# Performance work log

Hardware: AMD Instinct MI355X
Metric: run time of the kernel (lower is better)

Reference implementation:

```python
import jax, jax.numpy as jnp
import numpy as np

L, E, S, V, B, T = 6, 768, 1024, 32000, 2, 1024
FF = 4 * E
EPS = 1e-5

def _layernorm(v, w, b):
    m = jnp.mean(v, axis=-1, keepdims=True)
    var = jnp.mean((v - m) ** 2, axis=-1, keepdims=True)
    return (v - m) * jax.lax.rsqrt(var + EPS) * w + b

def setup_inputs() -> dict:
    key = jax.random.key(0)
    ks = jax.random.split(key, 12)
    s = 0.02
    n = lambda k, shp: (jax.random.normal(k, shp, jnp.float32) * s)
    return {
        "x": jax.random.randint(ks[0], (B, T), 0, V),
        "tok_emb": n(ks[1], (V, E)),
        "pos_emb": jax.random.normal(ks[2], (S, E), jnp.float32),  # nn.Parameter(randn)
        "Wq": n(ks[3], (L, E, E)), "bq": jnp.zeros((L, E), jnp.float32),
        "Wk": n(ks[4], (L, E, E)), "bk": jnp.zeros((L, E), jnp.float32),
        "Wv": n(ks[5], (L, E, E)), "bv": jnp.zeros((L, E), jnp.float32),
        "ln1w": jnp.ones((L, E), jnp.float32), "ln1b": jnp.zeros((L, E), jnp.float32),
        "W1": n(ks[6], (L, E, FF)), "b1": jnp.zeros((L, FF), jnp.float32),
        "W2": n(ks[7], (L, FF, E)), "b2": jnp.zeros((L, E), jnp.float32),
        "ln2w": jnp.ones((L, E), jnp.float32), "ln2b": jnp.zeros((L, E), jnp.float32),
        "Wo": n(ks[8], (E, V)), "bo": jnp.zeros((V,), jnp.float32),
    }

def reference(x, tok_emb, pos_emb, Wq, bq, Wk, bk, Wv, bv, ln1w, ln1b,
              W1, b1, W2, b2, ln2w, ln2b, Wo, bo):
    t = x.shape[1]
    h = tok_emb[x] + pos_emb[:t]  # [B,T,E]
    scale = jnp.sqrt(jnp.float32(E))
    tril = jnp.tril(jnp.ones((t, t), bool))

    def layer(h, p):
        wq, bq_, wk, bk_, wv, bv_, l1w, l1b, w1, b1_, w2, b2_, l2w, l2b = p
        Q = h @ wq + bq_
        K = h @ wk + bk_
        Vv = h @ wv + bv_
        scores = jnp.einsum('btd,bsd->bts', Q, K) / scale
        # original adds a mask of 1.0 on allowed positions, -inf elsewhere
        masked = jnp.where(tril, scores + 1.0, -jnp.inf)
        A = jax.nn.softmax(masked, axis=-1)
        att = jnp.einsum('bts,bsd->btd', A, Vv)
        h1 = _layernorm(h + att, l1w, l1b)
        ffn = jax.nn.relu(h1 @ w1 + b1_) @ w2 + b2_
        h2 = _layernorm(ffn + h1, l2w, l2b)
        return h2, None

    params = (Wq, bq, Wk, bk, Wv, bv, ln1w, ln1b, W1, b1, W2, b2, ln2w, ln2b)
    h, _ = jax.lax.scan(layer, h, params)
    return h @ Wo + bo  # [B,T,V]
```

## Files before the change

kernel.cpp:

```cpp
#include <hip/hip_runtime.h>
#include <stdint.h>

typedef __bf16 v8bf __attribute__((ext_vector_type(8)));
typedef float  v4f  __attribute__((ext_vector_type(4)));

__device__ __forceinline__ float bf2f(uint16_t h) {
    union { uint32_t u; float f; } x; x.u = ((uint32_t)h) << 16; return x.f;
}
__device__ __forceinline__ uint16_t f2bf(float f) {
    union { float f; uint32_t u; } x; x.f = f;
    uint32_t r = x.u + 0x7fffu + ((x.u >> 16) & 1u);
    return (uint16_t)(r >> 16);
}

__device__ __forceinline__ void gload16(const uint16_t* g, uint16_t* l) {
    __builtin_amdgcn_global_load_lds((const __attribute__((address_space(1))) void*)g,
                                     (__attribute__((address_space(3))) void*)l, 16, 0, 0);
}

__global__ void k_embed(const int* __restrict__ x, const float* __restrict__ tok,
                        const float* __restrict__ pos, float* __restrict__ hf,
                        uint16_t* __restrict__ hb)
{
    int i = blockIdx.x;
    int t = i & 1023;
    int tk = x[i];
    const float* te = tok + (long)tk * 768;
    const float* pe = pos + (long)t * 768;
    for (int j = threadIdx.x; j < 768; j += 256) {
        float v = te[j] + pe[j];
        hf[(long)i * 768 + j] = v;
        hb[(long)i * 768 + j] = f2bf(v);
    }
}

template<typename SrcT>
__global__ void k_transpose(const SrcT* __restrict__ src, uint16_t* __restrict__ dst,
                            int ldS, int ldD, long sBatch, long dBatch)
{
    __shared__ float tile[32][33];
    src += (long)blockIdx.z * sBatch;
    dst += (long)blockIdx.z * dBatch;
    int c0 = blockIdx.x * 32, r0 = blockIdx.y * 32;
    int tx = threadIdx.x, ty = threadIdx.y;
    #pragma unroll
    for (int i = 0; i < 4; ++i) {
        int r = r0 + ty + i * 8;
        SrcT s = src[(long)r * ldS + c0 + tx];
        float v;
        if constexpr (sizeof(SrcT) == 4) v = (float)s; else v = bf2f((uint16_t)s);
        tile[ty + i * 8][tx] = v;
    }
    __syncthreads();
    #pragma unroll
    for (int i = 0; i < 4; ++i) {
        int c = c0 + ty + i * 8;
        dst[(long)c * ldD + r0 + tx] = f2bf(tile[tx][ty + i * 8]);
    }
}

__global__ void k_concat3(const float* __restrict__ a, const float* __restrict__ b,
                          const float* __restrict__ c, float* __restrict__ out)
{
    int l = blockIdx.y;
    const float* s = (blockIdx.x == 0) ? a : ((blockIdx.x == 1) ? b : c);
    s += (long)l * 768;
    for (int j = threadIdx.x; j < 768; j += 256)
        out[(long)l * 2304 + blockIdx.x * 768 + j] = s[j];
}

template<typename OutT, int BN, bool BIAS, bool RELU, bool RES>
__global__ void k_gemm(const uint16_t* __restrict__ A, const uint16_t* __restrict__ BT,
                       OutT* __restrict__ C, const float* __restrict__ bias,
                       const float* __restrict__ res,
                       int K, int lda, int ldb, int ldc,
                       long bsA, long bsB, long bsC, float scale, int causal)
{
    constexpr int NT = BN / 32;
    const int nwg = gridDim.x * gridDim.y;
    int lin = blockIdx.y * gridDim.x + blockIdx.x;
    {
        int q = nwg >> 3, r = nwg & 7, x = lin & 7, i = lin >> 3;
        lin = (x < r ? x * (q + 1) : r * (q + 1) + (x - r) * q) + i;
    }
    const int mt = lin % gridDim.y;
    const int nt = lin / gridDim.y;

    if (causal == 1 && nt * BN >= (mt + 1) * 128) return;
    const int Keff = (causal == 2) ? ((mt + 1) * 128 < K ? (mt + 1) * 128 : K) : K;

    __shared__ uint16_t As[128 * 32];
    __shared__ uint16_t Bs[BN * 32];
    const int tid  = threadIdx.x;
    const int lane = tid & 63;
    const int bz   = blockIdx.z;
    const uint16_t* Ab = A + (long)bz * bsA + (long)mt * 128 * lda;
    const uint16_t* Bb = BT + (long)bz * bsB + (long)nt * BN * ldb;

    const int wm = (tid >> 6) >> 1, wn = (tid >> 6) & 1;
    const int fr = lane & 15, fq = lane >> 4;

    const int r0 = tid >> 2;
    const int s0 = (tid & 3) * 8;

    v4f acc[4][NT];
    #pragma unroll
    for (int m = 0; m < 4; ++m)
        #pragma unroll
        for (int n = 0; n < NT; ++n) acc[m][n] = (v4f){0.f, 0.f, 0.f, 0.f};

    for (int kt = 0; kt < Keff; kt += 32) {
        gload16(Ab + (long)r0 * lda + kt + s0,        &As[tid * 8]);
        gload16(Ab + (long)(r0 + 64) * lda + kt + s0, &As[2048 + tid * 8]);
        gload16(Bb + (long)r0 * ldb + kt + s0,        &Bs[tid * 8]);
        if constexpr (BN == 128)
            gload16(Bb + (long)(r0 + 64) * ldb + kt + s0, &Bs[2048 + tid * 8]);
        __syncthreads();
        v8bf ag[4], bg[NT];
        #pragma unroll
        for (int m = 0; m < 4; ++m)
            ag[m] = *(const v8bf*)&As[(wm * 64 + m * 16 + fr) * 32 + fq * 8];
        #pragma unroll
        for (int n = 0; n < NT; ++n)
            bg[n] = *(const v8bf*)&Bs[(wn * (BN / 2) + n * 16 + fr) * 32 + fq * 8];
        #pragma unroll
        for (int m = 0; m < 4; ++m)
            #pragma unroll
            for (int n = 0; n < NT; ++n)
                acc[m][n] = __builtin_amdgcn_mfma_f32_16x16x32_bf16(ag[m], bg[n], acc[m][n], 0, 0, 0);
        __syncthreads();
    }

    OutT* Cb = C + (long)bz * bsC + (long)mt * 128 * ldc + nt * BN;
    const float* Rb = RES ? (res + (long)bz * bsC + (long)mt * 128 * ldc + nt * BN) : nullptr;
    #pragma unroll
    for (int n = 0; n < NT; ++n) {
        int col = wn * (BN / 2) + n * 16 + fr;
        float bv = BIAS ? bias[nt * BN + col] : 0.f;
        #pragma unroll
        for (int m = 0; m < 4; ++m) {
            #pragma unroll
            for (int r = 0; r < 4; ++r) {
                int row = wm * 64 + m * 16 + fq * 4 + r;
                float v = acc[m][n][r] * scale + bv;
                if (RES) v += Rb[(long)row * ldc + col];
                if (RELU) v = fmaxf(v, 0.f);
                if constexpr (sizeof(OutT) == 4) Cb[(long)row * ldc + col] = v;
                else                             Cb[(long)row * ldc + col] = f2bf(v);
            }
        }
    }
}

__global__ __launch_bounds__(512, 2)
void k_gemm256(const uint16_t* __restrict__ A, const uint16_t* __restrict__ BT,
               float* __restrict__ C, const float* __restrict__ bias,
               int K, int lda, int ldb, int ldc, float scale)
{
    __shared__ uint16_t lds[4][2][8192];

    const int nwg = gridDim.x * gridDim.y;
    int lin = blockIdx.y * gridDim.x + blockIdx.x;
    {
        int q = nwg >> 3, r = nwg & 7, x = lin & 7, i = lin >> 3;
        lin = (x < r ? x * (q + 1) : r * (q + 1) + (x - r) * q) + i;
    }
    const int mt = lin % gridDim.y;
    const int nt = lin / gridDim.y;

    const int tid  = threadIdx.x;
    const int lane = tid & 63;
    const int wid  = tid >> 6;
    const int wm = wid >> 2, wn = wid & 3;
    const int fr = lane & 15, fq = lane >> 4;
    const int swz = (fq ^ (fr & 3)) * 8;

    const uint16_t* Ab = A  + (long)mt * 256 * lda;
    const uint16_t* Bb = BT + (long)nt * 256 * ldb;

    const int srow = tid >> 2;
    const int ssl  = ((tid & 3) ^ (srow & 3)) * 8;
    const int KT   = K >> 5;

    v4f acc[8][4];
    #pragma unroll
    for (int m = 0; m < 8; ++m)
        #pragma unroll
        for (int n = 0; n < 4; ++n) acc[m][n] = (v4f){0.f, 0.f, 0.f, 0.f};

    #pragma unroll
    for (int t = 0; t < 2; ++t) {
        gload16(Ab + (long)srow * lda + t * 32 + ssl,         &lds[t][0][tid * 8]);
        gload16(Ab + (long)(srow + 128) * lda + t * 32 + ssl, &lds[t][0][4096 + tid * 8]);
        gload16(Bb + (long)srow * ldb + t * 32 + ssl,         &lds[t][1][tid * 8]);
        gload16(Bb + (long)(srow + 128) * ldb + t * 32 + ssl, &lds[t][1][4096 + tid * 8]);
    }

    for (int kti = 0; kti < KT; ++kti) {
        const int ring = kti & 3;
        const uint16_t* lA = &lds[ring][0][0];
        const uint16_t* lB = &lds[ring][1][0];
        uint16_t* sA = &lds[(ring + 2) & 3][0][0];
        uint16_t* sB = &lds[(ring + 2) & 3][1][0];
        const int koff = (kti + 2) * 32;
        const bool more = (kti + 2) < KT;

        if (kti + 1 < KT) asm volatile("s_waitcnt vmcnt(4)" ::: "memory");
        else              asm volatile("s_waitcnt vmcnt(0)" ::: "memory");
        __builtin_amdgcn_s_barrier();

        v8bf bfr[4], a0[4];
        #pragma unroll
        for (int n = 0; n < 4; ++n)
            bfr[n] = *(const v8bf*)&lB[(wn * 64 + n * 16 + fr) * 32 + swz];
        #pragma unroll
        for (int m = 0; m < 4; ++m)
            a0[m] = *(const v8bf*)&lA[(wm * 128 + m * 16 + fr) * 32 + swz];
        if (more) {
            gload16(Ab + (long)srow * lda + koff + ssl,         &sA[tid * 8]);
            gload16(Ab + (long)(srow + 128) * lda + koff + ssl, &sA[4096 + tid * 8]);
        }
        __builtin_amdgcn_s_setprio(1);
        #pragma unroll
        for (int m = 0; m < 4; ++m)
            #pragma unroll
            for (int n = 0; n < 4; ++n)
                acc[m][n] = __builtin_amdgcn_mfma_f32_16x16x32_bf16(a0[m], bfr[n], acc[m][n], 0, 0, 0);
        __builtin_amdgcn_s_setprio(0);

        __builtin_amdgcn_s_barrier();
        v8bf a1[4];
        #pragma unroll
        for (int m = 0; m < 4; ++m)
            a1[m] = *(const v8bf*)&lA[(wm * 128 + (m + 4) * 16 + fr) * 32 + swz];
        if (more) {
            gload16(Bb + (long)srow * ldb + koff + ssl,         &sB[tid * 8]);
            gload16(Bb + (long)(srow + 128) * ldb + koff + ssl, &sB[4096 + tid * 8]);
        }
        __builtin_amdgcn_s_setprio(1);
        #pragma unroll
        for (int m = 0; m < 4; ++m)
            #pragma unroll
            for (int n = 0; n < 4; ++n)
                acc[m + 4][n] = __builtin_amdgcn_mfma_f32_16x16x32_bf16(a1[m], bfr[n], acc[m + 4][n], 0, 0, 0);
        __builtin_amdgcn_s_setprio(0);
    }

    float* Cb = C + (long)(mt * 256 + wm * 128) * ldc + nt * 256 + wn * 64;
    #pragma unroll
    for (int n = 0; n < 4; ++n) {
        int col = n * 16 + fr;
        float bv = bias[nt * 256 + wn * 64 + col];
        #pragma unroll
        for (int m = 0; m < 8; ++m) {
            #pragma unroll
            for (int r = 0; r < 4; ++r) {
                int row = m * 16 + fq * 4 + r;
                Cb[(long)row * ldc + col] = acc[m][n][r] * scale + bv;
            }
        }
    }
}

__global__ void k_softmax(const float* __restrict__ S, uint16_t* __restrict__ P)
{
    int t = blockIdx.x, b = blockIdx.y;
    const float* row = S + ((long)b * 1024 + t) * 1024;
    uint16_t* pr = P + ((long)b * 1024 + t) * 1024;
    int limit = (t & ~127) + 128;
    int s0 = threadIdx.x * 4;
    float vals[4] = {0.f, 0.f, 0.f, 0.f};
    if (s0 < limit) {
        float4 vv = *(const float4*)(row + s0);
        vals[0] = vv.x; vals[1] = vv.y; vals[2] = vv.z; vals[3] = vv.w;
    }
    float mx = -1e30f;
    #pragma unroll
    for (int j = 0; j < 4; ++j) if (s0 + j <= t) mx = fmaxf(mx, vals[j]);
    #pragma unroll
    for (int o = 32; o; o >>= 1) mx = fmaxf(mx, __shfl_xor(mx, o));
    __shared__ float red[8];
    int wave = threadIdx.x >> 6, lane = threadIdx.x & 63;
    if (lane == 0) red[wave] = mx;
    __syncthreads();
    mx = fmaxf(fmaxf(red[0], red[1]), fmaxf(red[2], red[3]));
    float e[4]; float sum = 0.f;
    #pragma unroll
    for (int j = 0; j < 4; ++j) { e[j] = (s0 + j <= t) ? __expf(vals[j] - mx) : 0.f; sum += e[j]; }
    #pragma unroll
    for (int o = 32; o; o >>= 1) sum += __shfl_xor(sum, o);
    if (lane == 0) red[4 + wave] = sum;
    __syncthreads();
    sum = red[4] + red[5] + red[6] + red[7];
    float inv = 1.f / sum;
    if (s0 < limit) {
        #pragma unroll
        for (int j = 0; j < 4; ++j) pr[s0 + j] = f2bf(e[j] * inv);
    }
}

__global__ void k_ln(const float* __restrict__ a,
                     const float* __restrict__ w, const float* __restrict__ bias,
                     float* __restrict__ outf, uint16_t* __restrict__ outb)
{
    int row = blockIdx.x;
    const float* ar = a + (long)row * 768;
    float v[3]; float s1 = 0.f, s2 = 0.f;
    #pragma unroll
    for (int i = 0; i < 3; ++i) {
        int e = threadIdx.x + i * 256;
        v[i] = ar[e];
        s1 += v[i]; s2 += v[i] * v[i];
    }
    #pragma unroll
    for (int o = 32; o; o >>= 1) { s1 += __shfl_xor(s1, o); s2 += __shfl_xor(s2, o); }
    __shared__ float red[8];
    int wave = threadIdx.x >> 6, lane = threadIdx.x & 63;
    if (lane == 0) { red[wave] = s1; red[4 + wave] = s2; }
    __syncthreads();
    s1 = red[0] + red[1] + red[2] + red[3];
    s2 = red[4] + red[5] + red[6] + red[7];
    float mean = s1 * (1.f / 768.f);
    float var  = s2 * (1.f / 768.f) - mean * mean;
    float rstd = rsqrtf(var + 1e-5f);
    #pragma unroll
    for (int i = 0; i < 3; ++i) {
        int e = threadIdx.x + i * 256;
        float o = (v[i] - mean) * rstd * w[e] + bias[e];
        outf[(long)row * 768 + e] = o;
        outb[(long)row * 768 + e] = f2bf(o);
    }
}

__global__ void k_ln_ffn2(const float* __restrict__ p, long pstride,
                          const float* __restrict__ b2, const float* __restrict__ h1,
                          const float* __restrict__ w, const float* __restrict__ bias,
                          float* __restrict__ outf, uint16_t* __restrict__ outb)
{
    int row = blockIdx.x;
    long base = (long)row * 768;
    float v[3]; float s1 = 0.f, s2 = 0.f;
    #pragma unroll
    for (int i = 0; i < 3; ++i) {
        int e = threadIdx.x + i * 256;
        float acc = b2[e] + h1[base + e];
        #pragma unroll
        for (int s = 0; s < 4; ++s) acc += p[base + e + s * pstride];
        v[i] = acc;
        s1 += acc; s2 += acc * acc;
    }
    #pragma unroll
    for (int o = 32; o; o >>= 1) { s1 += __shfl_xor(s1, o); s2 += __shfl_xor(s2, o); }
    __shared__ float red[8];
    int wave = threadIdx.x >> 6, lane = threadIdx.x & 63;
    if (lane == 0) { red[wave] = s1; red[4 + wave] = s2; }
    __syncthreads();
    s1 = red[0] + red[1] + red[2] + red[3];
    s2 = red[4] + red[5] + red[6] + red[7];
    float mean = s1 * (1.f / 768.f);
    float var  = s2 * (1.f / 768.f) - mean * mean;
    float rstd = rsqrtf(var + 1e-5f);
    #pragma unroll
    for (int i = 0; i < 3; ++i) {
        int e = threadIdx.x + i * 256;
        float o = (v[i] - mean) * rstd * w[e] + bias[e];
        outf[base + e] = o;
        outb[base + e] = f2bf(o);
    }
}

extern "C" void kernel_launch(void* const* d_in, const int* in_sizes, int n_in,
                              void* d_out, int out_size, void* d_ws, size_t ws_size,
                              hipStream_t stream)
{
    const int*   x       = (const int*)d_in[0];
    const float* tok_emb = (const float*)d_in[1];
    const float* pos_emb = (const float*)d_in[2];
    const float* Wq  = (const float*)d_in[3];
    const float* bq  = (const float*)d_in[4];
    const float* Wk  = (const float*)d_in[5];
    const float* bk  = (const float*)d_in[6];
    const float* Wv  = (const float*)d_in[7];
    const float* bv  = (const float*)d_in[8];
    const float* ln1w = (const float*)d_in[9];
    const float* ln1b = (const float*)d_in[10];
    const float* W1  = (const float*)d_in[11];
    const float* b1  = (const float*)d_in[12];
    const float* W2  = (const float*)d_in[13];
    const float* b2  = (const float*)d_in[14];
    const float* ln2w = (const float*)d_in[15];
    const float* ln2b = (const float*)d_in[16];
    const float* Wo  = (const float*)d_in[17];
    const float* bo  = (const float*)d_in[18];
    float* out = (float*)d_out;
    (void)in_sizes; (void)n_in; (void)out_size;

    char* ws = (char*)d_ws;
    size_t off = 0;
    auto alloc = [&](size_t bytes) -> char* {
        char* p = ws + off;
        off = (off + bytes + 255) & ~(size_t)255;
        return p;
    };
    uint16_t* WoT   = (uint16_t*)alloc(32000L * 768 * 2);
    float*    hf    = (float*)alloc(2048L * 768 * 4);
    uint16_t* hb    = (uint16_t*)alloc(2048L * 768 * 2);
    uint16_t* qkv   = (uint16_t*)alloc(2048L * 2304 * 2);
    uint16_t* vT    = (uint16_t*)alloc(2L * 768 * 1024 * 2);
    float*    sc    = (float*)alloc(2L * 1024 * 1024 * 4);
    uint16_t* pr    = (uint16_t*)alloc(2L * 1024 * 1024 * 2);
    float*    hsum  = (float*)alloc(2048L * 768 * 4);
    float*    h1f   = (float*)alloc(2048L * 768 * 4);
    uint16_t* h1b   = (uint16_t*)alloc(2048L * 768 * 2);
    uint16_t* f1    = (uint16_t*)alloc(2048L * 3072 * 2);
    float*    f2p   = (float*)alloc(4L * 2048 * 768 * 4);
    float*    bqkvA = (float*)alloc(6L * 2304 * 4);
    const long PSTR = 2048L * 768;

    size_t mark = off;
    uint16_t* WqkvTA = (uint16_t*)alloc(6L * 2304 * 768 * 2);
    uint16_t* W1TA   = (uint16_t*)alloc(6L * 3072 * 768 * 2);
    uint16_t* W2TA   = (uint16_t*)alloc(6L * 768 * 3072 * 2);
    bool hoist = (off <= ws_size);
    uint16_t *WqkvT = nullptr, *W1T = nullptr, *W2T = nullptr;
    if (!hoist) {
        off = mark;
        WqkvT = (uint16_t*)alloc(2304L * 768 * 2);
        W1T   = (uint16_t*)alloc(3072L * 768 * 2);
        W2T   = (uint16_t*)alloc(768L * 3072 * 2);
    }

    dim3 tb(32, 8);
    const float iscale = 0.036084391824351615f;
    const long EE = 768L * 768;

    k_transpose<float><<<dim3(1000, 24, 1), tb, 0, stream>>>(Wo, WoT, 32000, 768, 0, 0);
    k_embed<<<2048, 256, 0, stream>>>(x, tok_emb, pos_emb, hf, hb);
    k_concat3<<<dim3(3, 6), 256, 0, stream>>>(bq, bk, bv, bqkvA);

    if (hoist) {
        k_transpose<float><<<dim3(24, 24, 6), tb, 0, stream>>>(Wq, WqkvTA,             768, 768, EE, 2304L*768);
        k_transpose<float><<<dim3(24, 24, 6), tb, 0, stream>>>(Wk, WqkvTA + 768L*768,  768, 768, EE, 2304L*768);
        k_transpose<float><<<dim3(24, 24, 6), tb, 0, stream>>>(Wv, WqkvTA + 1536L*768, 768, 768, EE, 2304L*768);
        k_transpose<float><<<dim3(96, 24, 6), tb, 0, stream>>>(W1, W1TA, 3072, 768, 768L*3072, 3072L*768);
        k_transpose<float><<<dim3(24, 96, 6), tb, 0, stream>>>(W2, W2TA, 768, 3072, 3072L*768, 768L*3072);
    }

    for (int l = 0; l < 6; ++l) {
        uint16_t* WqkvL = hoist ? (WqkvTA + l * 2304L * 768) : WqkvT;
        uint16_t* W1L   = hoist ? (W1TA   + l * 3072L * 768) : W1T;
        uint16_t* W2L   = hoist ? (W2TA   + l * 768L * 3072) : W2T;
        if (!hoist) {
            k_transpose<float><<<dim3(24, 24, 1), tb, 0, stream>>>(Wq + l * EE, WqkvT,             768, 768, 0, 0);
            k_transpose<float><<<dim3(24, 24, 1), tb, 0, stream>>>(Wk + l * EE, WqkvT + 768L*768,  768, 768, 0, 0);
            k_transpose<float><<<dim3(24, 24, 1), tb, 0, stream>>>(Wv + l * EE, WqkvT + 1536L*768, 768, 768, 0, 0);
            k_transpose<float><<<dim3(96, 24, 1), tb, 0, stream>>>(W1 + l * 768L * 3072, W1T, 3072, 768, 0, 0);
            k_transpose<float><<<dim3(24, 96, 1), tb, 0, stream>>>(W2 + l * 3072L * 768, W2T, 768, 3072, 0, 0);
        }

        k_gemm<uint16_t, 64, true, false, false><<<dim3(36, 16, 1), 256, 0, stream>>>(
            hb, WqkvL, qkv, bqkvA + l * 2304, nullptr, 768, 768, 768, 2304, 0, 0, 0, 1.f, 0);
        k_gemm<float, 64, false, false, false><<<dim3(16, 8, 2), 256, 0, stream>>>(
            qkv, qkv + 768, sc, nullptr, nullptr, 768, 2304, 2304, 1024,
            1024L * 2304, 1024L * 2304, 1024L * 1024, iscale, 1);
        k_softmax<<<dim3(1024, 2), 256, 0, stream>>>(sc, pr);
        k_transpose<uint16_t><<<dim3(24, 32, 2), tb, 0, stream>>>(
            qkv + 1536, vT, 2304, 1024, 1024L * 2304, 768L * 1024);
        k_gemm<float, 64, false, false, true><<<dim3(12, 8, 2), 256, 0, stream>>>(
            pr, vT, hsum, nullptr, hf, 1024, 1024, 1024, 768,
            1024L * 1024, 768L * 1024, 1024L * 768, 1.f, 2);
        k_ln<<<2048, 256, 0, stream>>>(hsum, ln1w + l * 768, ln1b + l * 768, h1f, h1b);
        k_gemm<uint16_t, 64, true, true, false><<<dim3(48, 16, 1), 256, 0, stream>>>(
            h1b, W1L, f1, b1 + l * 3072, nullptr, 768, 768, 768, 3072, 0, 0, 0, 1.f, 0);
        k_gemm<float, 128, false, false, false><<<dim3(6, 16, 4), 256, 0, stream>>>(
            f1, W2L, f2p, nullptr, nullptr, 768, 3072, 3072, 768,
            768, 768, PSTR, 1.f, 0);
        k_ln_ffn2<<<2048, 256, 0, stream>>>(f2p, PSTR, b2 + l * 768, h1f,
                                            ln2w + l * 768, ln2b + l * 768, hf, hb);
    }

    k_gemm256<<<dim3(125, 8, 1), 512, 0, stream>>>(
        hb, WoT, out, bo, 768, 768, 768, 32000, 1.f);
}
```

Baseline: 962.9 us.

## Software-pipeline layer GEMMs with 4-stage LDS ring and deepen LM-head prefetch

Converts the per-layer GEMM from a synchronous load/sync/compute loop into a 4-slot LDS ring with prefetch distance 2. It uses direct global-to-LDS loads with swizzled slots, vmcnt waits and raised priority around the MFMAs. The big LM-head GEMM now prefetches three stages ahead, issues all loads once per iteration, and drops the mid-iteration barrier. The FFN2 launch switches from BN=128 to BN=64 with twice the blocks. This aims to hide global memory latency behind MFMA work. In exchange it uses more LDS per block, which may reduce occupancy, and relies on hand-counted vmcnt values being correct.

```diff
diff --git a/kernel.cpp b/kernel.cpp
--- a/kernel.cpp
+++ b/kernel.cpp
@@ -70,13 +70,14 @@
 }
 
 template<typename OutT, int BN, bool BIAS, bool RELU, bool RES>
-__global__ void k_gemm(const uint16_t* __restrict__ A, const uint16_t* __restrict__ BT,
-                       OutT* __restrict__ C, const float* __restrict__ bias,
-                       const float* __restrict__ res,
-                       int K, int lda, int ldb, int ldc,
-                       long bsA, long bsB, long bsC, float scale, int causal)
+__global__ void k_gemmp(const uint16_t* __restrict__ A, const uint16_t* __restrict__ BT,
+                        OutT* __restrict__ C, const float* __restrict__ bias,
+                        const float* __restrict__ res,
+                        int K, int lda, int ldb, int ldc,
+                        long bsA, long bsB, long bsC, float scale, int causal)
 {
     constexpr int NT = BN / 32;
+    constexpr int BOFF = 128 * 32;
     const int nwg = gridDim.x * gridDim.y;
     int lin = blockIdx.y * gridDim.x + blockIdx.x;
     {
@@ -88,9 +89,9 @@
 
     if (causal == 1 && nt * BN >= (mt + 1) * 128) return;
     const int Keff = (causal == 2) ? ((mt + 1) * 128 < K ? (mt + 1) * 128 : K) : K;
-
-    __shared__ uint16_t As[128 * 32];
-    __shared__ uint16_t Bs[BN * 32];
+    const int KT = Keff >> 5;
+
+    __shared__ uint16_t lds[4][(128 + BN) * 32];
     const int tid  = threadIdx.x;
     const int lane = tid & 63;
     const int bz   = blockIdx.z;
@@ -99,9 +100,10 @@
 
     const int wm = (tid >> 6) >> 1, wn = (tid >> 6) & 1;
     const int fr = lane & 15, fq = lane >> 4;
-
-    const int r0 = tid >> 2;
-    const int s0 = (tid & 3) * 8;
+    const int swz = (fq ^ (fr & 3)) * 8;
+
+    const int r0  = tid >> 2;
+    const int ssl = ((tid & 3) ^ (r0 & 3)) * 8;
 
     v4f acc[4][NT];
     #pragma unroll
@@ -109,26 +111,51 @@
         #pragma unroll
         for (int n = 0; n < NT; ++n) acc[m][n] = (v4f){0.f, 0.f, 0.f, 0.f};
 
-    for (int kt = 0; kt < Keff; kt += 32) {
-        gload16(Ab + (long)r0 * lda + kt + s0,        &As[tid * 8]);
-        gload16(Ab + (long)(r0 + 64) * lda + kt + s0, &As[2048 + tid * 8]);
-        gload16(Bb + (long)r0 * ldb + kt + s0,        &Bs[tid * 8]);
+    #pragma unroll
+    for (int t = 0; t < 2; ++t) {
+        gload16(Ab + (long)r0 * lda + t * 32 + ssl,        &lds[t][tid * 8]);
+        gload16(Ab + (long)(r0 + 64) * lda + t * 32 + ssl, &lds[t][2048 + tid * 8]);
+        gload16(Bb + (long)r0 * ldb + t * 32 + ssl,        &lds[t][BOFF + tid * 8]);
         if constexpr (BN == 128)
-            gload16(Bb + (long)(r0 + 64) * ldb + kt + s0, &Bs[2048 + tid * 8]);
-        __syncthreads();
+            gload16(Bb + (long)(r0 + 64) * ldb + t * 32 + ssl, &lds[t][BOFF + 2048 + tid * 8]);
+    }
+
+    for (int kti = 0; kti < KT; ++kti) {
+        if (kti < KT - 1) {
+            if constexpr (BN == 128) asm volatile("s_waitcnt vmcnt(4)" ::: "memory");
+            else                     asm volatile("s_waitcnt vmcnt(3)" ::: "memory");
+        } else {
+            asm volatile("s_waitcnt vmcnt(0)" ::: "memory");
+        }
+        __builtin_amdgcn_s_barrier();
+
+        const uint16_t* lA = &lds[kti & 3][0];
+        const uint16_t* lB = &lds[kti & 3][BOFF];
         v8bf ag[4], bg[NT];
         #pragma unroll
         for (int m = 0; m < 4; ++m)
-            ag[m] = *(const v8bf*)&As[(wm * 64 + m * 16 + fr) * 32 + fq * 8];
+            ag[m] = *(const v8bf*)&lA[(wm * 64 + m * 16 + fr) * 32 + swz];
         #pragma unroll
         for (int n = 0; n < NT; ++n)
-            bg[n] = *(const v8bf*)&Bs[(wn * (BN / 2) + n * 16 + fr) * 32 + fq * 8];
+            bg[n] = *(const v8bf*)&lB[(wn * (BN / 2) + n * 16 + fr) * 32 + swz];
+
+        if (kti + 2 < KT) {
+            const int ko = (kti + 2) * 32;
+            uint16_t* s = &lds[(kti + 2) & 3][0];
+            gload16(Ab + (long)r0 * lda + ko + ssl,        &s[tid * 8]);
+            gload16(Ab + (long)(r0 + 64) * lda + ko + ssl, &s[2048 + tid * 8]);
+            gload16(Bb + (long)r0 * ldb + ko + ssl,        &s[BOFF + tid * 8]);
+            if constexpr (BN == 128)
+                gload16(Bb + (long)(r0 + 64) * ldb + ko + ssl, &s[BOFF + 2048 + tid * 8]);
+        }
+
+        __builtin_amdgcn_s_setprio(1);
         #pragma unroll
         for (int m = 0; m < 4; ++m)
             #pragma unroll
             for (int n = 0; n < NT; ++n)
                 acc[m][n] = __builtin_amdgcn_mfma_f32_16x16x32_bf16(ag[m], bg[n], acc[m][n], 0, 0, 0);
-        __syncthreads();
+        __builtin_amdgcn_s_setprio(0);
     }
 
     OutT* Cb = C + (long)bz * bsC + (long)mt * 128 * ldc + nt * BN;
@@ -189,7 +216,7 @@
         for (int n = 0; n < 4; ++n) acc[m][n] = (v4f){0.f, 0.f, 0.f, 0.f};
 
     #pragma unroll
-    for (int t = 0; t < 2; ++t) {
+    for (int t = 0; t < 3; ++t) {
         gload16(Ab + (long)srow * lda + t * 32 + ssl,         &lds[t][0][tid * 8]);
         gload16(Ab + (long)(srow + 128) * lda + t * 32 + ssl, &lds[t][0][4096 + tid * 8]);
         gload16(Bb + (long)srow * ldb + t * 32 + ssl,         &lds[t][1][tid * 8]);
@@ -197,47 +224,41 @@
     }
 
     for (int kti = 0; kti < KT; ++kti) {
+        if (kti < KT - 2)      asm volatile("s_waitcnt vmcnt(8)" ::: "memory");
+        else if (kti == KT - 2) asm volatile("s_waitcnt vmcnt(4)" ::: "memory");
+        else                    asm volatile("s_waitcnt vmcnt(0)" ::: "memory");
+        __builtin_amdgcn_s_barrier();
+
         const int ring = kti & 3;
         const uint16_t* lA = &lds[ring][0][0];
         const uint16_t* lB = &lds[ring][1][0];
-        uint16_t* sA = &lds[(ring + 2) & 3][0][0];
-        uint16_t* sB = &lds[(ring + 2) & 3][1][0];
-        const int koff = (kti + 2) * 32;
-        const bool more = (kti + 2) < KT;
-
-        if (kti + 1 < KT) asm volatile("s_waitcnt vmcnt(4)" ::: "memory");
-        else              asm volatile("s_waitcnt vmcnt(0)" ::: "memory");
-        __builtin_amdgcn_s_barrier();
-
-        v8bf bfr[4], a0[4];
+
+        v8bf bfr[4], a0[4], a1[4];
         #pragma unroll
         for (int n = 0; n < 4; ++n)
             bfr[n] = *(const v8bf*)&lB[(wn * 64 + n * 16 + fr) * 32 + swz];
         #pragma unroll
-        for (int m = 0; m < 4; ++m)
+        for (int m = 0; m < 4; ++m) {
             a0[m] = *(const v8bf*)&lA[(wm * 128 + m * 16 + fr) * 32 + swz];
-        if (more) {
-            gload16(Ab + (long)srow * lda + koff + ssl,         &sA[tid * 8]);
-            gload16(Ab + (long)(srow + 128) * lda + koff + ssl, &sA[4096 + tid * 8]);
-        }
+            a1[m] = *(const v8bf*)&lA[(wm * 128 + (m + 4) * 16 + fr) * 32 + swz];
+        }
+
+        if (kti + 3 < KT) {
+            const int ko = (kti + 3) * 32;
+            uint16_t* sA = &lds[(kti + 3) & 3][0][0];
+            uint16_t* sB = &lds[(kti + 3) & 3][1][0];
+            gload16(Ab + (long)srow * lda + ko + ssl,         &sA[tid * 8]);
+            gload16(Ab + (long)(srow + 128) * lda + ko + ssl, &sA[4096 + tid * 8]);
+            gload16(Bb + (long)srow * ldb + ko + ssl,         &sB[tid * 8]);
+            gload16(Bb + (long)(srow + 128) * ldb + ko + ssl, &sB[4096 + tid * 8]);
+        }
+
         __builtin_amdgcn_s_setprio(1);
         #pragma unroll
         for (int m = 0; m < 4; ++m)
             #pragma unroll
             for (int n = 0; n < 4; ++n)
                 acc[m][n] = __builtin_amdgcn_mfma_f32_16x16x32_bf16(a0[m], bfr[n], acc[m][n], 0, 0, 0);
-        __builtin_amdgcn_s_setprio(0);
-
-        __builtin_amdgcn_s_barrier();
-        v8bf a1[4];
-        #pragma unroll
-        for (int m = 0; m < 4; ++m)
-            a1[m] = *(const v8bf*)&lA[(wm * 128 + (m + 4) * 16 + fr) * 32 + swz];
-        if (more) {
-            gload16(Bb + (long)srow * ldb + koff + ssl,         &sB[tid * 8]);
-            gload16(Bb + (long)(srow + 128) * ldb + koff + ssl, &sB[4096 + tid * 8]);
-        }
-        __builtin_amdgcn_s_setprio(1);
         #pragma unroll
         for (int m = 0; m < 4; ++m)
             #pragma unroll
@@ -458,21 +479,21 @@
             k_transpose<float><<<dim3(24, 96, 1), tb, 0, stream>>>(W2 + l * 3072L * 768, W2T, 768, 3072, 0, 0);
         }
 
-        k_gemm<uint16_t, 64, true, false, false><<<dim3(36, 16, 1), 256, 0, stream>>>(
+        k_gemmp<uint16_t, 64, true, false, false><<<dim3(36, 16, 1), 256, 0, stream>>>(
             hb, WqkvL, qkv, bqkvA + l * 2304, nullptr, 768, 768, 768, 2304, 0, 0, 0, 1.f, 0);
-        k_gemm<float, 64, false, false, false><<<dim3(16, 8, 2), 256, 0, stream>>>(
+        k_gemmp<float, 64, false, false, false><<<dim3(16, 8, 2), 256, 0, stream>>>(
             qkv, qkv + 768, sc, nullptr, nullptr, 768, 2304, 2304, 1024,
             1024L * 2304, 1024L * 2304, 1024L * 1024, iscale, 1);
         k_softmax<<<dim3(1024, 2), 256, 0, stream>>>(sc, pr);
         k_transpose<uint16_t><<<dim3(24, 32, 2), tb, 0, stream>>>(
             qkv + 1536, vT, 2304, 1024, 1024L * 2304, 768L * 1024);
-        k_gemm<float, 64, false, false, true><<<dim3(12, 8, 2), 256, 0, stream>>>(
+        k_gemmp<float, 64, false, false, true><<<dim3(12, 8, 2), 256, 0, stream>>>(
             pr, vT, hsum, nullptr, hf, 1024, 1024, 1024, 768,
             1024L * 1024, 768L * 1024, 1024L * 768, 1.f, 2);
         k_ln<<<2048, 256, 0, stream>>>(hsum, ln1w + l * 768, ln1b + l * 768, h1f, h1b);
-        k_gemm<uint16_t, 64, true, true, false><<<dim3(48, 16, 1), 256, 0, stream>>>(
+        k_gemmp<uint16_t, 64, true, true, false><<<dim3(48, 16, 1), 256, 0, stream>>>(
             h1b, W1L, f1, b1 + l * 3072, nullptr, 768, 768, 768, 3072, 0, 0, 0, 1.f, 0);
-        k_gemm<float, 128, false, false, false><<<dim3(6, 16, 4), 256, 0, stream>>>(
+        k_gemmp<float, 64, false, false, false><<<dim3(12, 16, 4), 256, 0, stream>>>(
             f1, W2L, f2p, nullptr, nullptr, 768, 3072, 3072, 768,
             768, 768, PSTR, 1.f, 0);
         k_ln_ffn2<<<2048, 256, 0, stream>>>(f2p, PSTR, b2 + l * 768, h1f,
```

After: 884.2 us. -8.2%, faster.

## Double-buffer GEMM K-loops with 64-wide swizzled LDS tiles and nontemporal logits stores

Applied to the files above, without the earlier changes.

Rewrites the layer GEMM as a double-buffered kernel with BK=64 and XOR-swizzled LDS. The next tile's global-to-LDS load is issued right after the barrier so it overlaps the MFMAs, and MFMA priority is raised. The FFN2 GEMM drops from BN=128 to a fixed BN=64 with a doubled grid. The logits GEMM moves from a 4-deep BK=32 ring to a 2-buffer BK=64 scheme and writes its large fp32 output with nontemporal stores. The aim is fewer barriers and better overlap of loads with compute, at the cost of more LDS per block and a shallower prefetch for the logits kernel.

```diff
diff --git a/kernel.cpp b/kernel.cpp
--- a/kernel.cpp
+++ b/kernel.cpp
@@ -69,14 +69,14 @@
         out[(long)l * 2304 + blockIdx.x * 768 + j] = s[j];
 }
 
-template<typename OutT, int BN, bool BIAS, bool RELU, bool RES>
-__global__ void k_gemm(const uint16_t* __restrict__ A, const uint16_t* __restrict__ BT,
-                       OutT* __restrict__ C, const float* __restrict__ bias,
-                       const float* __restrict__ res,
-                       int K, int lda, int ldb, int ldc,
-                       long bsA, long bsB, long bsC, float scale, int causal)
-{
-    constexpr int NT = BN / 32;
+template<typename OutT, bool BIAS, bool RELU, bool RES>
+__global__ __launch_bounds__(256, 3)
+void k_gemmp(const uint16_t* __restrict__ A, const uint16_t* __restrict__ BT,
+             OutT* __restrict__ C, const float* __restrict__ bias,
+             const float* __restrict__ res,
+             int K, int lda, int ldb, int ldc,
+             long bsA, long bsB, long bsC, float scale, int causal)
+{
     const int nwg = gridDim.x * gridDim.y;
     int lin = blockIdx.y * gridDim.x + blockIdx.x;
     {
@@ -86,57 +86,79 @@
     const int mt = lin % gridDim.y;
     const int nt = lin / gridDim.y;
 
-    if (causal == 1 && nt * BN >= (mt + 1) * 128) return;
+    if (causal == 1 && nt * 64 >= (mt + 1) * 128) return;
     const int Keff = (causal == 2) ? ((mt + 1) * 128 < K ? (mt + 1) * 128 : K) : K;
-
-    __shared__ uint16_t As[128 * 32];
-    __shared__ uint16_t Bs[BN * 32];
+    const int KT = Keff >> 6;
+
+    __shared__ uint16_t lds[2][192 * 64];
     const int tid  = threadIdx.x;
     const int lane = tid & 63;
     const int bz   = blockIdx.z;
     const uint16_t* Ab = A + (long)bz * bsA + (long)mt * 128 * lda;
-    const uint16_t* Bb = BT + (long)bz * bsB + (long)nt * BN * ldb;
+    const uint16_t* Bb = BT + (long)bz * bsB + (long)nt * 64 * ldb;
 
     const int wm = (tid >> 6) >> 1, wn = (tid >> 6) & 1;
     const int fr = lane & 15, fq = lane >> 4;
 
-    const int r0 = tid >> 2;
-    const int s0 = (tid & 3) * 8;
-
-    v4f acc[4][NT];
+    const int srow = tid >> 3;
+    const int sl   = tid & 7;
+
+    v4f acc[4][2];
     #pragma unroll
     for (int m = 0; m < 4; ++m)
         #pragma unroll
-        for (int n = 0; n < NT; ++n) acc[m][n] = (v4f){0.f, 0.f, 0.f, 0.f};
-
-    for (int kt = 0; kt < Keff; kt += 32) {
-        gload16(Ab + (long)r0 * lda + kt + s0,        &As[tid * 8]);
-        gload16(Ab + (long)(r0 + 64) * lda + kt + s0, &As[2048 + tid * 8]);
-        gload16(Bb + (long)r0 * ldb + kt + s0,        &Bs[tid * 8]);
-        if constexpr (BN == 128)
-            gload16(Bb + (long)(r0 + 64) * ldb + kt + s0, &Bs[2048 + tid * 8]);
-        __syncthreads();
-        v8bf ag[4], bg[NT];
-        #pragma unroll
-        for (int m = 0; m < 4; ++m)
-            ag[m] = *(const v8bf*)&As[(wm * 64 + m * 16 + fr) * 32 + fq * 8];
-        #pragma unroll
-        for (int n = 0; n < NT; ++n)
-            bg[n] = *(const v8bf*)&Bs[(wn * (BN / 2) + n * 16 + fr) * 32 + fq * 8];
-        #pragma unroll
-        for (int m = 0; m < 4; ++m)
-            #pragma unroll
-            for (int n = 0; n < NT; ++n)
-                acc[m][n] = __builtin_amdgcn_mfma_f32_16x16x32_bf16(ag[m], bg[n], acc[m][n], 0, 0, 0);
-        __syncthreads();
-    }
-
-    OutT* Cb = C + (long)bz * bsC + (long)mt * 128 * ldc + nt * BN;
-    const float* Rb = RES ? (res + (long)bz * bsC + (long)mt * 128 * ldc + nt * BN) : nullptr;
-    #pragma unroll
-    for (int n = 0; n < NT; ++n) {
-        int col = wn * (BN / 2) + n * 16 + fr;
-        float bv = BIAS ? bias[nt * BN + col] : 0.f;
+        for (int n = 0; n < 2; ++n) acc[m][n] = (v4f){0.f, 0.f, 0.f, 0.f};
+
+    auto stage = [&](int t, int buf) {
+        const int ko = t * 64;
+        #pragma unroll
+        for (int p = 0; p < 6; ++p) {
+            int row = p * 32 + srow;
+            int ss  = (sl ^ (row & 7)) * 8;
+            const uint16_t* g = (p < 4) ? (Ab + (long)row * lda + ko + ss)
+                                        : (Bb + (long)(row - 128) * ldb + ko + ss);
+            gload16(g, &lds[buf][p * 2048 + tid * 8]);
+        }
+    };
+
+    stage(0, 0);
+
+    for (int kti = 0; kti < KT; ++kti) {
+        asm volatile("s_waitcnt vmcnt(0)" ::: "memory");
+        __builtin_amdgcn_s_barrier();
+        if (kti + 1 < KT) stage(kti + 1, (kti + 1) & 1);
+
+        const uint16_t* l = &lds[kti & 1][0];
+        #pragma unroll
+        for (int kk = 0; kk < 2; ++kk) {
+            const int sIdx = kk * 4 + fq;
+            v8bf ag[4], bg[2];
+            #pragma unroll
+            for (int m = 0; m < 4; ++m) {
+                int r = wm * 64 + m * 16 + fr;
+                ag[m] = *(const v8bf*)&l[r * 64 + ((sIdx ^ (r & 7)) << 3)];
+            }
+            #pragma unroll
+            for (int n = 0; n < 2; ++n) {
+                int r = 128 + wn * 32 + n * 16 + fr;
+                bg[n] = *(const v8bf*)&l[r * 64 + ((sIdx ^ (r & 7)) << 3)];
+            }
+            __builtin_amdgcn_s_setprio(1);
+            #pragma unroll
+            for (int m = 0; m < 4; ++m)
+                #pragma unroll
+                for (int n = 0; n < 2; ++n)
+                    acc[m][n] = __builtin_amdgcn_mfma_f32_16x16x32_bf16(ag[m], bg[n], acc[m][n], 0, 0, 0);
+            __builtin_amdgcn_s_setprio(0);
+        }
+    }
+
+    OutT* Cb = C + (long)bz * bsC + (long)mt * 128 * ldc + nt * 64;
+    const float* Rb = RES ? (res + (long)bz * bsC + (long)mt * 128 * ldc + nt * 64) : nullptr;
+    #pragma unroll
+    for (int n = 0; n < 2; ++n) {
+        int col = wn * 32 + n * 16 + fr;
+        float bv = BIAS ? bias[nt * 64 + col] : 0.f;
         #pragma unroll
         for (int m = 0; m < 4; ++m) {
             #pragma unroll
@@ -153,11 +175,11 @@
 }
 
 __global__ __launch_bounds__(512, 2)
-void k_gemm256(const uint16_t* __restrict__ A, const uint16_t* __restrict__ BT,
+void k_glogits(const uint16_t* __restrict__ A, const uint16_t* __restrict__ BT,
                float* __restrict__ C, const float* __restrict__ bias,
                int K, int lda, int ldb, int ldc, float scale)
 {
-    __shared__ uint16_t lds[4][2][8192];
+    __shared__ uint16_t lds[2][512 * 64];
 
     const int nwg = gridDim.x * gridDim.y;
     int lin = blockIdx.y * gridDim.x + blockIdx.x;
@@ -173,14 +195,13 @@
     const int wid  = tid >> 6;
     const int wm = wid >> 2, wn = wid & 3;
     const int fr = lane & 15, fq = lane >> 4;
-    const int swz = (fq ^ (fr & 3)) * 8;
 
     const uint16_t* Ab = A  + (long)mt * 256 * lda;
     const uint16_t* Bb = BT + (long)nt * 256 * ldb;
 
-    const int srow = tid >> 2;
-    const int ssl  = ((tid & 3) ^ (srow & 3)) * 8;
-    const int KT   = K >> 5;
+    const int srow = tid >> 3;
+    const int sl   = tid & 7;
+    const int KT   = K >> 6;
 
     v4f acc[8][4];
     #pragma unroll
@@ -188,62 +209,48 @@
         #pragma unroll
         for (int n = 0; n < 4; ++n) acc[m][n] = (v4f){0.f, 0.f, 0.f, 0.f};
 
-    #pragma unroll
-    for (int t = 0; t < 2; ++t) {
-        gload16(Ab + (long)srow * lda + t * 32 + ssl,         &lds[t][0][tid * 8]);
-        gload16(Ab + (long)(srow + 128) * lda + t * 32 + ssl, &lds[t][0][4096 + tid * 8]);
-        gload16(Bb + (long)srow * ldb + t * 32 + ssl,         &lds[t][1][tid * 8]);
-        gload16(Bb + (long)(srow + 128) * ldb + t * 32 + ssl, &lds[t][1][4096 + tid * 8]);
-    }
+    auto stage = [&](int t, int buf) {
+        const int ko = t * 64;
+        #pragma unroll
+        for (int p = 0; p < 8; ++p) {
+            int row = p * 64 + srow;
+            int ss  = (sl ^ (row & 7)) * 8;
+            const uint16_t* g = (p < 4) ? (Ab + (long)row * lda + ko + ss)
+                                        : (Bb + (long)(row - 256) * ldb + ko + ss);
+            gload16(g, &lds[buf][p * 4096 + tid * 8]);
+        }
+    };
+
+    stage(0, 0);
 
     for (int kti = 0; kti < KT; ++kti) {
-        const int ring = kti & 3;
-        const uint16_t* lA = &lds[ring][0][0];
-        const uint16_t* lB = &lds[ring][1][0];
-        uint16_t* sA = &lds[(ring + 2) & 3][0][0];
-        uint16_t* sB = &lds[(ring + 2) & 3][1][0];
-        const int koff = (kti + 2) * 32;
-        const bool more = (kti + 2) < KT;
-
-        if (kti + 1 < KT) asm volatile("s_waitcnt vmcnt(4)" ::: "memory");
-        else              asm volatile("s_waitcnt vmcnt(0)" ::: "memory");
+        asm volatile("s_waitcnt vmcnt(0)" ::: "memory");
         __builtin_amdgcn_s_barrier();
-
-        v8bf bfr[4], a0[4];
-        #pragma unroll
-        for (int n = 0; n < 4; ++n)
-            bfr[n] = *(const v8bf*)&lB[(wn * 64 + n * 16 + fr) * 32 + swz];
-        #pragma unroll
-        for (int m = 0; m < 4; ++m)
-            a0[m] = *(const v8bf*)&lA[(wm * 128 + m * 16 + fr) * 32 + swz];
-        if (more) {
-            gload16(Ab + (long)srow * lda + koff + ssl,         &sA[tid * 8]);
-            gload16(Ab + (long)(srow + 128) * lda + koff + ssl, &sA[4096 + tid * 8]);
-        }
-        __builtin_amdgcn_s_setprio(1);
-        #pragma unroll
-        for (int m = 0; m < 4; ++m)
-            #pragma unroll
-            for (int n = 0; n < 4; ++n)
-                acc[m][n] = __builtin_amdgcn_mfma_f32_16x16x32_bf16(a0[m], bfr[n], acc[m][n], 0, 0, 0);
-        __builtin_amdgcn_s_setprio(0);
-
-        __builtin_amdgcn_s_barrier();
-        v8bf a1[4];
-        #pragma unroll
-        for (int m = 0; m < 4; ++m)
-            a1[m] = *(const v8bf*)&lA[(wm * 128 + (m + 4) * 16 + fr) * 32 + swz];
-        if (more) {
-            gload16(Bb + (long)srow * ldb + koff + ssl,         &sB[tid * 8]);
-            gload16(Bb + (long)(srow + 128) * ldb + koff + ssl, &sB[4096 + tid * 8]);
-        }
-        __builtin_amdgcn_s_setprio(1);
-        #pragma unroll
-        for (int m = 0; m < 4; ++m)
-            #pragma unroll
-            for (int n = 0; n < 4; ++n)
-                acc[m + 4][n] = __builtin_amdgcn_mfma_f32_16x16x32_bf16(a1[m], bfr[n], acc[m + 4][n], 0, 0, 0);
-        __builtin_amdgcn_s_setprio(0);
+        if (kti + 1 < KT) stage(kti + 1, (kti + 1) & 1);
+
+        const uint16_t* l = &lds[kti & 1][0];
+        #pragma unroll
+        for (int kk = 0; kk < 2; ++kk) {
+            const int sIdx = kk * 4 + fq;
+            v8bf ag[8], bg[4];
+            #pragma unroll
+            for (int m = 0; m < 8; ++m) {
+                int r = wm * 128 + m * 16 + fr;
+                ag[m] = *(const v8bf*)&l[r * 64 + ((sIdx ^ (r & 7)) << 3)];
+            }
+            #pragma unroll
+            for (int n = 0; n < 4; ++n) {
+                int r = 256 + wn * 64 + n * 16 + fr;
+                bg[n] = *(const v8bf*)&l[r * 64 + ((sIdx ^ (r & 7)) << 3)];
+            }
+            __builtin_amdgcn_s_setprio(1);
+            #pragma unroll
+            for (int m = 0; m < 8; ++m)
+                #pragma unroll
+                for (int n = 0; n < 4; ++n)
+                    acc[m][n] = __builtin_amdgcn_mfma_f32_16x16x32_bf16(ag[m], bg[n], acc[m][n], 0, 0, 0);
+            __builtin_amdgcn_s_setprio(0);
+        }
     }
 
     float* Cb = C + (long)(mt * 256 + wm * 128) * ldc + nt * 256 + wn * 64;
@@ -256,7 +263,7 @@
             #pragma unroll
             for (int r = 0; r < 4; ++r) {
                 int row = m * 16 + fq * 4 + r;
-                Cb[(long)row * ldc + col] = acc[m][n][r] * scale + bv;
+                __builtin_nontemporal_store(acc[m][n][r] * scale + bv, &Cb[(long)row * ldc + col]);
             }
         }
     }
@@ -458,27 +465,27 @@
             k_transpose<float><<<dim3(24, 96, 1), tb, 0, stream>>>(W2 + l * 3072L * 768, W2T, 768, 3072, 0, 0);
         }
 
-        k_gemm<uint16_t, 64, true, false, false><<<dim3(36, 16, 1), 256, 0, stream>>>(
+        k_gemmp<uint16_t, true, false, false><<<dim3(36, 16, 1), 256, 0, stream>>>(
             hb, WqkvL, qkv, bqkvA + l * 2304, nullptr, 768, 768, 768, 2304, 0, 0, 0, 1.f, 0);
-        k_gemm<float, 64, false, false, false><<<dim3(16, 8, 2), 256, 0, stream>>>(
+        k_gemmp<float, false, false, false><<<dim3(16, 8, 2), 256, 0, stream>>>(
             qkv, qkv + 768, sc, nullptr, nullptr, 768, 2304, 2304, 1024,
             1024L * 2304, 1024L * 2304, 1024L * 1024, iscale, 1);
         k_softmax<<<dim3(1024, 2), 256, 0, stream>>>(sc, pr);
         k_transpose<uint16_t><<<dim3(24, 32, 2), tb, 0, stream>>>(
             qkv + 1536, vT, 2304, 1024, 1024L * 2304, 768L * 1024);
-        k_gemm<float, 64, false, false, true><<<dim3(12, 8, 2), 256, 0, stream>>>(
+        k_gemmp<float, false, false, true><<<dim3(12, 8, 2), 256, 0, stream>>>(
             pr, vT, hsum, nullptr, hf, 1024, 1024, 1024, 768,
             1024L * 1024, 768L * 1024, 1024L * 768, 1.f, 2);
         k_ln<<<2048, 256, 0, stream>>>(hsum, ln1w + l * 768, ln1b + l * 768, h1f, h1b);
-        k_gemm<uint16_t, 64, true, true, false><<<dim3(48, 16, 1), 256, 0, stream>>>(
+        k_gemmp<uint16_t, true, true, false><<<dim3(48, 16, 1), 256, 0, stream>>>(
             h1b, W1L, f1, b1 + l * 3072, nullptr, 768, 768, 768, 3072, 0, 0, 0, 1.f, 0);
-        k_gemm<float, 128, false, false, false><<<dim3(6, 16, 4), 256, 0, stream>>>(
+        k_gemmp<float, false, false, false><<<dim3(12, 16, 4), 256, 0, stream>>>(
             f1, W2L, f2p, nullptr, nullptr, 768, 3072, 3072, 768,
             768, 768, PSTR, 1.f, 0);
         k_ln_ffn2<<<2048, 256, 0, stream>>>(f2p, PSTR, b2 + l * 768, h1f,
                                             ln2w + l * 768, ln2b + l * 768, hf, hb);
     }
 
-    k_gemm256<<<dim3(125, 8, 1), 512, 0, stream>>>(
+    k_glogits<<<dim3(125, 8, 1), 512, 0, stream>>>(
         hb, WoT, out, bo, 768, 768, 768, 32000, 1.f);
 }
```

New measurement: 822.8 us. 14.6% less time.
